# Performance work log

Hardware: AMD Instinct MI355X
Metric: run time of the kernel (lower is better)

The kernel has to match this reference:

```python
import jax, jax.numpy as jnp
import numpy as np

DENSE_SHAPE = (256, 3, 3, 256)  # (out_channels, kh, kw, in_channels)
STRIDES = (1, 1)


def _unfold_nchw(x, kh, kw, sh, sw):
    """torch.nn.functional.unfold layout: rows ordered (C, kh, kw)."""
    B, C, H, W = x.shape
    oh = (H - kh) // sh + 1
    ow = (W - kw) // sw + 1
    # [B, C, kh*kw, oh, ow]; small python loop over 3x3 kernel taps only
    patches = jnp.stack(
        [x[:, :, i:i + sh * oh:sh, j:j + sw * ow:sw]
         for i in range(kh) for j in range(kw)], axis=2)
    return patches.reshape(B, C * kh * kw, oh * ow), oh, ow


def setup_inputs() -> dict:
    key = jax.random.key(0)
    k1, k2, k3, k4, k5, k6 = jax.random.split(key, 6)
    O, kh, kw, C = DENSE_SHAPE
    nnz = 2048
    inp = jax.random.normal(k1, (4, 128, 128, C), dtype=jnp.float32)
    # per-column index ranges for COO weight indices [nnz, 4]
    io = jax.random.randint(k2, (nnz, 1), 0, O)
    ih = jax.random.randint(k3, (nnz, 1), 0, kh)
    iw = jax.random.randint(k4, (nnz, 1), 0, kw)
    ic = jax.random.randint(k5, (nnz, 1), 0, C)
    weight_indices = jnp.concatenate([io, ih, iw, ic], axis=1).astype(jnp.int64)
    weight_values = jax.random.normal(k6, (nnz,), dtype=jnp.float32)
    return {"input": inp, "weight_indices": weight_indices,
            "weight_values": weight_values}


def reference(input, weight_indices, weight_values):
    O, kh, kw, C = DENSE_SHAPE
    sh, sw = STRIDES
    B = input.shape[0]
    # densify COO weight (duplicates are summed, matching coalesce)
    W = jnp.zeros(DENSE_SHAPE, dtype=weight_values.dtype).at[
        weight_indices[:, 0], weight_indices[:, 1],
        weight_indices[:, 2], weight_indices[:, 3]].add(weight_values)
    x = jnp.transpose(input, (0, 3, 1, 2))  # NHWC -> NCHW
    U, oh, ow = _unfold_nchw(x, kh, kw, sh, sw)  # [B, C*kh*kw, oh*ow]
    # NOTE: faithful to the original: weight flattened in (kh,kw,C) order
    # while unfold rows are in (C,kh,kw) order -- same raw matmul.
    out = jnp.einsum('ok,bkl->bol', W.reshape(O, -1), U)
    out = out.reshape(B, O, oh, ow)
    return jnp.transpose(out, (0, 2, 3, 1))  # -> NHWC
```

## Files before the change

kernel.cpp:

```cpp
#include <hip/hip_runtime.h>
#include <cstdint>

#define H_IN   128
#define W_IN   128
#define C_IN   256
#define O_OUT  256
#define OH     126
#define OW     126

#define TY     8
#define TX     8
#define IR     (TY + 2)
#define ICOLS  (TX + 2)
#define NPIX   (IR * ICOLS)
#define COLB   516
#define ROWB   5264
#define IN_BYTES (9 * ROWB + 9 * COLB + COLB)
#define NWAVES 16
#define OPW    16
#define SST    18
#define STG_W  (64 * SST)
#define FLUSH_BYTES (8 * STG_W * 4)
#define LDS_BYTES IN_BYTES

__global__ void prep_kernel(const int* __restrict__ wi, const float* __restrict__ wv,
                            int nnz, int* __restrict__ sgS, int* __restrict__ sgBase,
                            int2* __restrict__ tab) {
    __shared__ int cnt[256];
    __shared__ int smax[32];
    __shared__ int sbase[33];
    __shared__ int is32;
    const int tid = threadIdx.x;
    cnt[tid] = 0;
    if (tid == 0) is32 = 0;
    __syncthreads();
    int f = 0;
    for (int idx = tid * 2 + 1; idx < nnz * 4; idx += 512) f |= wi[idx];
    if (f) atomicOr(&is32, 1);
    __syncthreads();
    const int stride = is32 ? 4 : 8;
    const int step   = is32 ? 1 : 2;
    for (int e = tid; e < nnz; e += 256)
        atomicAdd(&cnt[wi[e * stride]], 1);
    __syncthreads();
    if (tid < 32) {
        int m = 0;
        for (int k = 0; k < 8; ++k) m = max(m, cnt[tid * 8 + k]);
        smax[tid] = m;
    }
    __syncthreads();
    if (tid == 0) {
        int s = 0;
        for (int i = 0; i < 32; ++i) { sbase[i] = s; s += 8 * smax[i]; }
        sbase[32] = s;
    }
    __syncthreads();
    const int T = sbase[32];
    for (int i = tid; i < T; i += 256) tab[i] = make_int2(0, 0);
    cnt[tid] = 0;
    __syncthreads();
    for (int e = tid; e < nnz; e += 256) {
        int o  = wi[e * stride];
        int h  = wi[e * stride + 1 * step];
        int w_ = wi[e * stride + 2 * step];
        int c  = wi[e * stride + 3 * step];
        int k   = h * 768 + w_ * 256 + c;
        int cp  = k / 9;
        int rem = k - cp * 9;
        int i_  = rem / 3;
        int j_  = rem - i_ * 3;
        int meta2 = i_ * ROWB + j_ * COLB + cp * 2;
        int slot = atomicAdd(&cnt[o], 1);
        tab[sbase[o >> 3] + slot * 8 + (o & 7)] = make_int2(meta2, __float_as_int(wv[e]));
    }
    if (tid < 32) sgS[tid] = smax[tid];
    if (tid < 33) sgBase[tid] = sbase[tid];
}

__device__ inline unsigned short rtne_bf16(float f) {
    unsigned u = __float_as_uint(f);
    u += 0x7FFFu + ((u >> 16) & 1u);
    return (unsigned short)(u >> 16);
}

__device__ __forceinline__ float bfld(const char* b, int off) {
    return __uint_as_float(((unsigned)*(const unsigned short*)(b + off)) << 16);
}

__global__ __launch_bounds__(1024, 8)
void conv_kernel(const float* __restrict__ in, float* __restrict__ out,
                 const int* __restrict__ sgS, const int* __restrict__ sgBase,
                 const int2* __restrict__ tab) {
    extern __shared__ char smem[];
    float* ldsF = (float*)smem;

    const int tid  = threadIdx.x;
    const int w    = __builtin_amdgcn_readfirstlane(tid >> 6);
    const int lane = tid & 63;
    const int tx = blockIdx.x, ty = blockIdx.y, b = blockIdx.z;
    const int iy0 = ty * TY, ix0 = tx * TX;
    const float* inb = in + (size_t)b * (H_IN * W_IN * C_IN);

    for (int base = 0; base < 8; base += 4) {
        float4 v[4];
#pragma unroll
        for (int q = 0; q < 4; ++q) {
            int p = w + (base + q) * NWAVES;
            if (p < NPIX) {
                int r = p / ICOLS, c = p - r * ICOLS;
                int gy = iy0 + r, gx = ix0 + c;
                if (gy < H_IN && gx < W_IN)
                    v[q] = *(const float4*)(inb + ((gy * W_IN + gx) << 8) + (lane << 2));
            }
        }
#pragma unroll
        for (int q = 0; q < 4; ++q) {
            int p = w + (base + q) * NWAVES;
            if (p < NPIX) {
                int r = p / ICOLS, c = p - r * ICOLS;
                int gy = iy0 + r, gx = ix0 + c;
                if (gy < H_IN && gx < W_IN) {
                    ushort2 lo, hi;
                    lo.x = rtne_bf16(v[q].x); lo.y = rtne_bf16(v[q].y);
                    hi.x = rtne_bf16(v[q].z); hi.y = rtne_bf16(v[q].w);
                    unsigned short* d = (unsigned short*)(smem + r * ROWB + c * COLB) + (lane << 2);
                    *(ushort2*)(d)     = lo;
                    *(ushort2*)(d + 2) = hi;
                }
            }
        }
    }
    __syncthreads();

    const int A2  = (lane >> 3) * ROWB + (lane & 7) * COLB;
    const int sgb = w * 2;
    const char* basep = (const char*)smem;
    float acc[OPW];
#pragma unroll
    for (int i = 0; i < OPW; ++i) acc[i] = 0.f;

#pragma unroll
    for (int g = 0; g < 2; ++g) {
        const int S = sgS[sgb + g];
        const int2* Tg = tab + sgBase[sgb + g];
        for (int slot = 0; slot < S; ++slot) {
            const int4* R = (const int4*)(Tg + (slot << 3));
            const int4 p0 = R[0];
            const int4 p1 = R[1];
            const int4 p2 = R[2];
            const int4 p3 = R[3];
            acc[g * 8 + 0] += __int_as_float(p0.y) * bfld(basep, A2 + p0.x);
            acc[g * 8 + 1] += __int_as_float(p0.w) * bfld(basep, A2 + p0.z);
            acc[g * 8 + 2] += __int_as_float(p1.y) * bfld(basep, A2 + p1.x);
            acc[g * 8 + 3] += __int_as_float(p1.w) * bfld(basep, A2 + p1.z);
            acc[g * 8 + 4] += __int_as_float(p2.y) * bfld(basep, A2 + p2.x);
            acc[g * 8 + 5] += __int_as_float(p2.w) * bfld(basep, A2 + p2.z);
            acc[g * 8 + 6] += __int_as_float(p3.y) * bfld(basep, A2 + p3.x);
            acc[g * 8 + 7] += __int_as_float(p3.w) * bfld(basep, A2 + p3.z);
        }
    }

    __syncthreads();
    const int ob = w * OPW;
    const int wq = w & 7;
    if (w < 8) {
        float* st = ldsF + wq * STG_W + lane * SST;
#pragma unroll
        for (int k = 0; k < OPW; k += 2)
            *(float2*)(st + k) = make_float2(acc[k], acc[k + 1]);
    }
    __syncthreads();
    if (w < 8) {
        const int a_  = lane >> 2;
        const int chq = lane & 3;
        const float* rb = ldsF + wq * STG_W;
#pragma unroll
        for (int s16 = 0; s16 < 4; ++s16) {
            int p = s16 * 16 + a_;
            float2 u0 = *(const float2*)(rb + p * SST + chq * 4);
            float2 u1 = *(const float2*)(rb + p * SST + chq * 4 + 2);
            int poy = iy0 + (p >> 3), pox = ix0 + (p & 7);
            if (poy < OH && pox < OW) {
                float4 o4 = make_float4(u0.x, u0.y, u1.x, u1.y);
                *(float4*)(out + (((size_t)b * OH + poy) * OW + pox) * O_OUT + ob + chq * 4) = o4;
            }
        }
    }
    __syncthreads();
    if (w >= 8) {
        float* st = ldsF + wq * STG_W + lane * SST;
#pragma unroll
        for (int k = 0; k < OPW; k += 2)
            *(float2*)(st + k) = make_float2(acc[k], acc[k + 1]);
    }
    __syncthreads();
    if (w >= 8) {
        const int a_  = lane >> 2;
        const int chq = lane & 3;
        const float* rb = ldsF + wq * STG_W;
#pragma unroll
        for (int s16 = 0; s16 < 4; ++s16) {
            int p = s16 * 16 + a_;
            float2 u0 = *(const float2*)(rb + p * SST + chq * 4);
            float2 u1 = *(const float2*)(rb + p * SST + chq * 4 + 2);
            int poy = iy0 + (p >> 3), pox = ix0 + (p & 7);
            if (poy < OH && pox < OW) {
                float4 o4 = make_float4(u0.x, u0.y, u1.x, u1.y);
                *(float4*)(out + (((size_t)b * OH + poy) * OW + pox) * O_OUT + ob + chq * 4) = o4;
            }
        }
    }
}

extern "C" void kernel_launch(void* const* d_in, const int* in_sizes, int n_in,
                              void* d_out, int out_size, void* d_ws, size_t ws_size,
                              hipStream_t stream) {
    const float* input = (const float*)d_in[0];
    const int*   widx  = (const int*)d_in[1];
    const float* wval  = (const float*)d_in[2];
    float* outp = (float*)d_out;
    const int nnz = in_sizes[2];
    const int B = in_sizes[0] / (H_IN * W_IN * C_IN);

    int*  sgS    = (int*)d_ws;
    int*  sgBase = sgS + 32;
    int2* tab    = (int2*)((char*)d_ws + 512);

    prep_kernel<<<1, 256, 0, stream>>>(widx, wval, nnz, sgS, sgBase, tab);

    static_assert(LDS_BYTES >= FLUSH_BYTES, "flush pass must fit in input region");
    static_assert(2 * LDS_BYTES <= 160 * 1024, "need 2 blocks/CU");
    hipFuncSetAttribute((const void*)conv_kernel,
                        hipFuncAttributeMaxDynamicSharedMemorySize, LDS_BYTES);
    dim3 grid((OW + TX - 1) / TX, (OH + TY - 1) / TY, B);
    conv_kernel<<<grid, 1024, LDS_BYTES, stream>>>(input, outp, sgS, sgBase, tab);
}
```

Baseline: 142.6 us.

## Sort output channels by nnz count and pair heavy/light groups per wave

The prep kernel now counting-sorts output channels by descending nonzero count, so each group of 8 channels has similar lengths and less padding in the slot table. Each wave then takes one heavy group and one light group (g and 31-g), which balances per-wave loop trip counts. A permutation array is written and used in the conv kernel to scatter accumulators back to their true channel positions in LDS before the coalesced output store. The cost is a more complex prep step and scalar, per-element scattered LDS writes in the flush.

Result: no change. 140.9 us (-1.2%).

```diff
diff --git a/kernel.cpp b/kernel.cpp
--- a/kernel.cpp
+++ b/kernel.cpp
@@ -25,13 +25,19 @@
 
 __global__ void prep_kernel(const int* __restrict__ wi, const float* __restrict__ wv,
                             int nnz, int* __restrict__ sgS, int* __restrict__ sgBase,
-                            int2* __restrict__ tab) {
+                            int* __restrict__ perm, int2* __restrict__ tab) {
     __shared__ int cnt[256];
+    __shared__ int ipos[256];
+    __shared__ int prm[256];
+    __shared__ int hist[64];
+    __shared__ int hbase[65];
+    __shared__ int hcur[64];
     __shared__ int smax[32];
     __shared__ int sbase[33];
     __shared__ int is32;
     const int tid = threadIdx.x;
     cnt[tid] = 0;
+    if (tid < 64) { hist[tid] = 0; hcur[tid] = 0; }
     if (tid == 0) is32 = 0;
     __syncthreads();
     int f = 0;
@@ -43,9 +49,21 @@
     for (int e = tid; e < nnz; e += 256)
         atomicAdd(&cnt[wi[e * stride]], 1);
     __syncthreads();
+    { int key = 63 - min(cnt[tid], 63); atomicAdd(&hist[key], 1); }
+    __syncthreads();
+    if (tid == 0) {
+        int s = 0;
+        for (int i = 0; i < 64; ++i) { hbase[i] = s; s += hist[i]; }
+        hbase[64] = s;
+    }
+    __syncthreads();
+    { int key = 63 - min(cnt[tid], 63);
+      int pos = hbase[key] + atomicAdd(&hcur[key], 1);
+      ipos[tid] = pos; prm[pos] = tid; }
+    __syncthreads();
     if (tid < 32) {
         int m = 0;
-        for (int k = 0; k < 8; ++k) m = max(m, cnt[tid * 8 + k]);
+        for (int k = 0; k < 8; ++k) m = max(m, cnt[prm[tid * 8 + k]]);
         smax[tid] = m;
     }
     __syncthreads();
@@ -71,10 +89,12 @@
         int j_  = rem - i_ * 3;
         int meta2 = i_ * ROWB + j_ * COLB + cp * 2;
         int slot = atomicAdd(&cnt[o], 1);
-        tab[sbase[o >> 3] + slot * 8 + (o & 7)] = make_int2(meta2, __float_as_int(wv[e]));
+        int p    = ipos[o];
+        tab[sbase[p >> 3] + slot * 8 + (p & 7)] = make_int2(meta2, __float_as_int(wv[e]));
     }
     if (tid < 32) sgS[tid] = smax[tid];
     if (tid < 33) sgBase[tid] = sbase[tid];
+    perm[tid] = prm[tid];
 }
 
 __device__ inline unsigned short rtne_bf16(float f) {
@@ -90,7 +110,7 @@
 __global__ __launch_bounds__(1024, 8)
 void conv_kernel(const float* __restrict__ in, float* __restrict__ out,
                  const int* __restrict__ sgS, const int* __restrict__ sgBase,
-                 const int2* __restrict__ tab) {
+                 const int* __restrict__ perm, const int2* __restrict__ tab) {
     extern __shared__ char smem[];
     float* ldsF = (float*)smem;
 
@@ -133,7 +153,7 @@
     __syncthreads();
 
     const int A2  = (lane >> 3) * ROWB + (lane & 7) * COLB;
-    const int sgb = w * 2;
+    const int g0 = w, g1 = 31 - w;
     const char* basep = (const char*)smem;
     float acc[OPW];
 #pragma unroll
@@ -141,8 +161,9 @@
 
 #pragma unroll
     for (int g = 0; g < 2; ++g) {
-        const int S = sgS[sgb + g];
-        const int2* Tg = tab + sgBase[sgb + g];
+        const int gi = g ? g1 : g0;
+        const int S = sgS[gi];
+        const int2* Tg = tab + sgBase[gi];
         for (int slot = 0; slot < S; ++slot) {
             const int4* R = (const int4*)(Tg + (slot << 3));
             const int4 p0 = R[0];
@@ -161,19 +182,24 @@
     }
 
     __syncthreads();
+    int tcs[OPW];
+#pragma unroll
+    for (int k = 0; k < OPW; ++k) {
+        const int grp = (k < 8) ? g0 : g1;
+        tcs[k] = perm[grp * 8 + (k & 7)];
+    }
     const int ob = w * OPW;
-    const int wq = w & 7;
-    if (w < 8) {
-        float* st = ldsF + wq * STG_W + lane * SST;
-#pragma unroll
-        for (int k = 0; k < OPW; k += 2)
-            *(float2*)(st + k) = make_float2(acc[k], acc[k + 1]);
+#pragma unroll
+    for (int k = 0; k < OPW; ++k) {
+        const int tc = tcs[k];
+        if ((tc >> 7) == 0)
+            ldsF[((tc >> 4) & 7) * STG_W + lane * SST + (tc & 15)] = acc[k];
     }
     __syncthreads();
     if (w < 8) {
         const int a_  = lane >> 2;
         const int chq = lane & 3;
-        const float* rb = ldsF + wq * STG_W;
+        const float* rb = ldsF + w * STG_W;
 #pragma unroll
         for (int s16 = 0; s16 < 4; ++s16) {
             int p = s16 * 16 + a_;
@@ -187,17 +213,17 @@
         }
     }
     __syncthreads();
-    if (w >= 8) {
-        float* st = ldsF + wq * STG_W + lane * SST;
-#pragma unroll
-        for (int k = 0; k < OPW; k += 2)
-            *(float2*)(st + k) = make_float2(acc[k], acc[k + 1]);
+#pragma unroll
+    for (int k = 0; k < OPW; ++k) {
+        const int tc = tcs[k];
+        if ((tc >> 7) == 1)
+            ldsF[((tc >> 4) & 7) * STG_W + lane * SST + (tc & 15)] = acc[k];
     }
     __syncthreads();
     if (w >= 8) {
         const int a_  = lane >> 2;
         const int chq = lane & 3;
-        const float* rb = ldsF + wq * STG_W;
+        const float* rb = ldsF + (w & 7) * STG_W;
 #pragma unroll
         for (int s16 = 0; s16 < 4; ++s16) {
             int p = s16 * 16 + a_;
@@ -224,14 +250,15 @@
 
     int*  sgS    = (int*)d_ws;
     int*  sgBase = sgS + 32;
-    int2* tab    = (int2*)((char*)d_ws + 512);
-
-    prep_kernel<<<1, 256, 0, stream>>>(widx, wval, nnz, sgS, sgBase, tab);
+    int*  perm   = (int*)((char*)d_ws + 512);
+    int2* tab    = (int2*)((char*)d_ws + 2048);
+
+    prep_kernel<<<1, 256, 0, stream>>>(widx, wval, nnz, sgS, sgBase, perm, tab);
 
     static_assert(LDS_BYTES >= FLUSH_BYTES, "flush pass must fit in input region");
     static_assert(2 * LDS_BYTES <= 160 * 1024, "need 2 blocks/CU");
     hipFuncSetAttribute((const void*)conv_kernel,
                         hipFuncAttributeMaxDynamicSharedMemorySize, LDS_BYTES);
     dim3 grid((OW + TX - 1) / TX, (OH + TY - 1) / TY, B);
-    conv_kernel<<<grid, 1024, LDS_BYTES, stream>>>(input, outp, sgS, sgBase, tab);
-}
+    conv_kernel<<<grid, 1024, LDS_BYTES, stream>>>(input, outp, sgS, sgBase, perm, tab);
+}
```
